# Optimization experiments

Hardware: AMD Instinct MI355X
Metric: run time of the kernel (lower is better)

The kernel has to match this reference:

```python
import jax, jax.numpy as jnp
import numpy as np

DIM = 1024
HEADS = 8
HEAD_DIM = DIM // HEADS
TAU = HEAD_DIM ** 0.5
BS, SEQ = 1, 2048


def setup_inputs() -> dict:
    key = jax.random.key(0)
    kq, kk, kv, kb = jax.random.split(key, 4)
    q = jax.random.normal(kq, (BS, SEQ, DIM), jnp.float32)
    k = jax.random.normal(kk, (BS, SEQ, DIM), jnp.float32)
    v = jax.random.normal(kv, (BS, SEQ, DIM), jnp.float32)
    Wi_w = jnp.zeros((HEADS, 3 * DIM), jnp.float32)
    Wi_b = 0.1 * jax.random.normal(kb, (HEADS,), jnp.float32)
    Wf_w = jnp.zeros((HEADS, 3 * DIM), jnp.float32)
    Wf_b = jnp.linspace(3.0, 6.0, HEADS, dtype=jnp.float32)  # equidistant_bias_init(3, 6)
    gn_w = jnp.ones((DIM,), jnp.float32)
    gn_b = jnp.zeros((DIM,), jnp.float32)
    return {"q": q, "k": k, "v": v, "Wi_w": Wi_w, "Wi_b": Wi_b,
            "Wf_w": Wf_w, "Wf_b": Wf_b, "gn_w": gn_w, "gn_b": gn_b}


def reference(q, k, v, Wi_w, Wi_b, Wf_w, Wf_b, gn_w, gn_b):
    bs, seq, dim = q.shape
    gate_in = jnp.concatenate([q, k, v], axis=-1)                    # [b, s, 3d]
    itilde = jnp.einsum('bsd,hd->bhs', gate_in, Wi_w) + Wi_b[None, :, None]
    ftilde = jnp.einsum('bsd,hd->bhs', gate_in, Wf_w) + Wf_b[None, :, None]

    # Decay matrix: F_act[i,j] = sum_{t=j+1..i} logsigmoid(ftilde_t), lower-tri else -inf
    csum = jnp.cumsum(jax.nn.log_sigmoid(ftilde), axis=-1)           # [b, h, s]
    Fmat = csum[..., :, None] - csum[..., None, :]                   # [b, h, s, s]
    mask = jnp.tril(jnp.ones((seq, seq), dtype=bool))
    F_act = jnp.where(mask, Fmat, -jnp.inf)

    Dtilde = F_act + itilde[..., None, :]                            # add input gate along j
    max_d = jnp.max(Dtilde, axis=-1, keepdims=True)
    D = jnp.exp(Dtilde - max_d)                                      # stabilized decay weights

    qh = q.reshape(bs, seq, HEADS, HEAD_DIM).transpose(0, 2, 1, 3)
    kh = k.reshape(bs, seq, HEADS, HEAD_DIM).transpose(0, 2, 1, 3)
    vh = v.reshape(bs, seq, HEADS, HEAD_DIM).transpose(0, 2, 1, 3)

    Ctilde = jnp.einsum('bhid,bhjd->bhij', qh, kh) * D / TAU
    maxit = jnp.maximum(jnp.abs(jnp.sum(Ctilde, axis=-1, keepdims=True)), jnp.exp(-max_d))
    Htilde = jnp.einsum('bhij,bhjd->bhid', Ctilde, vh) / (maxit + 1e-6)

    # GroupNorm(HEADS groups) over dim, applied per token
    x = Htilde.transpose(0, 2, 1, 3).reshape(bs * seq, HEADS, HEAD_DIM)
    mean = jnp.mean(x, axis=-1, keepdims=True)
    var = jnp.var(x, axis=-1, keepdims=True)
    xn = (x - mean) / jnp.sqrt(var + 1e-5)
    out = xn.reshape(bs * seq, DIM) * gn_w + gn_b
    return out.reshape(bs, seq, DIM)
```

## Files before the change

kernel.cpp:

```cpp
#include <hip/hip_runtime.h>
#include <math.h>

#define SEQ 2048
#define NH 8
#define HD 128
#define DIMF 1024
#define LOG2E 1.4426950408889634f
#define INVTAU 0.08838834764831845f

typedef __attribute__((ext_vector_type(8))) short bf16x8;
typedef __attribute__((ext_vector_type(8))) unsigned short us8;
typedef __attribute__((ext_vector_type(4))) float f32x4;
typedef __attribute__((ext_vector_type(16))) float f32x16;

__device__ float g_itacc[NH*SEQ];
__device__ float g_ftacc[NH*SEQ];
__device__ float g_aL[NH*SEQ];
__device__ float g_cmL[NH*SEQ];
__device__ float g_en[NH*SEQ];
__device__ unsigned short g_Qb[NH*SEQ*HD];
__device__ unsigned short g_Kb[NH*SEQ*HD];
__device__ unsigned short g_Vb[NH*SEQ*HD];
__device__ unsigned short g_Vt[NH*HD*SEQ];
__device__ unsigned short g_Wb[16*3072];

__device__ __forceinline__ unsigned short f2bf(float x) {
  unsigned u = __float_as_uint(x);
  u += 0x7fffu + ((u >> 16) & 1u);
  return (unsigned short)(u >> 16);
}

__device__ __forceinline__ unsigned packbf(float lo, float hi) {
  return (unsigned)f2bf(lo) | ((unsigned)f2bf(hi) << 16);
}

__global__ __launch_bounds__(256) void convert_kernel(const float* __restrict__ q,
                                                      const float* __restrict__ k,
                                                      const float* __restrict__ v,
                                                      const float* __restrict__ Wi,
                                                      const float* __restrict__ Wf) {
  const int bid = blockIdx.x;
  if (bid < 6144) {
    const int s = bid & 2047;
    const int t = bid >> 11;
    const float* src = (t == 0) ? q : (t == 1) ? k : v;
    unsigned short* dst = (t == 0) ? g_Qb : (t == 1) ? g_Kb : g_Vb;
    const int c = threadIdx.x * 4;
    const float4 f = *(const float4*)(src + s*DIMF + c);
    const int h = c >> 7, d = c & 127;
    ushort4 u;
    u.x = f2bf(f.x); u.y = f2bf(f.y); u.z = f2bf(f.z); u.w = f2bf(f.w);
    *(ushort4*)(dst + (h*SEQ + s)*HD + d) = u;
  } else {
    const int gid = (bid - 6144) * 256 + threadIdx.x;
    const int e4 = gid * 4;
    const int p = e4 / 3072;
    const int c = e4 % 3072;
    const float* src = (p < 8) ? (Wi + p*3072 + c) : (Wf + (p-8)*3072 + c);
    const float4 f = *(const float4*)src;
    ushort4 u;
    u.x = f2bf(f.x); u.y = f2bf(f.y); u.z = f2bf(f.z); u.w = f2bf(f.w);
    *(ushort4*)(g_Wb + p*3072 + c) = u;
  }
}

__global__ __launch_bounds__(256) void vtrans_kernel() {
  __shared__ __align__(16) unsigned short Ts[64*72];
  const int h  = blockIdx.x;
  const int s0 = blockIdx.y * 64;
  const int d0 = blockIdx.z * 64;
  const int t = threadIdx.x;
  {
    const int sr = t >> 2;
    const int c  = (t & 3) * 16;
    const unsigned short* src = g_Vb + (h*SEQ + s0 + sr)*HD + d0 + c;
    *(us8*)&Ts[sr*72 + c]     = *(const us8*)&src[0];
    *(us8*)&Ts[sr*72 + c + 8] = *(const us8*)&src[8];
  }
  __syncthreads();
  {
    const int w = t >> 6, l = t & 63;
    unsigned short outv[16];
    #pragma unroll
    for (int j = 0; j < 16; ++j) outv[j] = Ts[(w*16 + j)*72 + l];
    unsigned short* dst = g_Vt + (h*HD + d0 + l)*SEQ + s0 + w*16;
    *(us8*)&dst[0] = *(us8*)&outv[0];
    *(us8*)&dst[8] = *(us8*)&outv[8];
  }
}

__global__ __launch_bounds__(256) void gates_kernel() {
  __shared__ f32x4 red[4][64];
  const int tid = threadIdx.x;
  const int wave = tid >> 6, lane = tid & 63;
  const int q4 = lane >> 4, l16 = lane & 15;
  const int s0 = blockIdx.x * 16;
  f32x4 acc = {0.f, 0.f, 0.f, 0.f};
  #pragma unroll 8
  for (int ks = wave*24; ks < wave*24 + 24; ++ks) {
    const int k0 = ks*32 + q4*8;
    const int tsel = k0 >> 10;
    const int rem = k0 & 1023;
    const int hh = rem >> 7, dd = rem & 127;
    const unsigned short* base = (tsel == 0) ? g_Qb : (tsel == 1) ? g_Kb : g_Vb;
    const bf16x8 a = *(const bf16x8*)&base[(hh*SEQ + s0 + l16)*HD + dd];
    const bf16x8 b = *(const bf16x8*)&g_Wb[l16*3072 + k0];
    acc = __builtin_amdgcn_mfma_f32_16x16x32_bf16(a, b, acc, 0, 0, 0);
  }
  red[wave][lane] = acc;
  __syncthreads();
  if (wave == 0) {
    f32x4 s = red[0][lane];
    #pragma unroll
    for (int w = 1; w < 4; ++w) s += red[w][lane];
    #pragma unroll
    for (int r = 0; r < 4; ++r) {
      const int sg = s0 + 4*q4 + r;
      if (l16 < 8) g_itacc[l16*SEQ + sg] = s[r];
      else         g_ftacc[(l16-8)*SEQ + sg] = s[r];
    }
  }
}

__global__ __launch_bounds__(256) void scan_kernel(const float* __restrict__ Wi_b,
                                                   const float* __restrict__ Wf_b) {
  __shared__ float Wsum[4];
  __shared__ float Wmax[4];
  const int h = blockIdx.x;
  const int t = threadIdx.x;
  const int wave = t >> 6, lane = t & 63;
  const float ib = Wi_b[h];
  const float fb = Wf_b[h];
  const int base = h*SEQ + t*8;

  float it[8], ft[8];
  *(float4*)&it[0] = *(const float4*)&g_itacc[base];
  *(float4*)&it[4] = *(const float4*)&g_itacc[base+4];
  *(float4*)&ft[0] = *(const float4*)&g_ftacc[base];
  *(float4*)&ft[4] = *(const float4*)&g_ftacc[base+4];

  float cs[8];
  float run = 0.f;
  #pragma unroll
  for (int j = 0; j < 8; ++j) {
    const float f = ft[j] + fb;
    const float ls = fminf(f, 0.f) - log1pf(expf(-fabsf(f)));
    run += ls;
    cs[j] = run;
  }
  float x = run;
  #pragma unroll
  for (int off = 1; off < 64; off <<= 1) {
    const float tv = __shfl_up(x, off, 64);
    if (lane >= off) x += tv;
  }
  const float wexcl = x - run;
  if (lane == 63) Wsum[wave] = x;
  __syncthreads();
  float boff = 0.f;
  #pragma unroll
  for (int w = 0; w < 4; ++w) if (w < wave) boff += Wsum[w];
  const float cbase = boff + wexcl;

  float a[8], am[8], csum[8];
  float m = -__builtin_inff();
  #pragma unroll
  for (int j = 0; j < 8; ++j) {
    csum[j] = cbase + cs[j];
    a[j] = (it[j] + ib) - csum[j];
    m = fmaxf(m, a[j]);
    am[j] = m;
  }
  float y = m;
  #pragma unroll
  for (int off = 1; off < 64; off <<= 1) {
    const float tv = __shfl_up(y, off, 64);
    if (lane >= off) y = fmaxf(y, tv);
  }
  float e = __shfl_up(y, 1, 64);
  if (lane == 0) e = -__builtin_inff();
  if (lane == 63) Wmax[wave] = y;
  __syncthreads();
  float bmax = -__builtin_inff();
  #pragma unroll
  for (int w = 0; w < 4; ++w) if (w < wave) bmax = fmaxf(bmax, Wmax[w]);
  const float pre = fmaxf(bmax, e);

  float oa[8], ocm[8], oen[8];
  #pragma unroll
  for (int j = 0; j < 8; ++j) {
    const float cm = fmaxf(pre, am[j]);
    oa[j]  = a[j] * LOG2E;
    ocm[j] = cm * LOG2E;
    oen[j] = expf(-(csum[j] + cm));
  }
  *(float4*)&g_aL[base]    = *(float4*)&oa[0];
  *(float4*)&g_aL[base+4]  = *(float4*)&oa[4];
  *(float4*)&g_cmL[base]   = *(float4*)&ocm[0];
  *(float4*)&g_cmL[base+4] = *(float4*)&ocm[4];
  *(float4*)&g_en[base]    = *(float4*)&oen[0];
  *(float4*)&g_en[base+4]  = *(float4*)&oen[4];
}

__global__ __launch_bounds__(256, 1) void attn_kernel(const float* __restrict__ gnw,
                                                      const float* __restrict__ gnb,
                                                      float* __restrict__ out) {
  __shared__ float Osum[2][32][132];
  __shared__ float Sred[4][32];

  const int h = blockIdx.x;
  const int y = blockIdx.y;
  const int tS = y, tB = 63 - y;
  const int iS0 = 32*tS, iB0 = 32*tB;
  const int iSmax = iS0 + 31, iBmax = iB0 + 31;
  const int nvB = tB/4 + 1;

  const int tid  = threadIdx.x;
  const int w    = tid >> 6;
  const int lane = tid & 63;
  const int l31  = lane & 31;
  const int hi   = lane >> 5;

  const unsigned short* Kgh = g_Kb + (h*SEQ + l31)*HD + hi*8;
  const unsigned short* Vgh = g_Vt + (h*HD + l31)*SEQ + hi*8;
  const float*          aLh = g_aL + h*SEQ + 4*hi;

  bf16x8 qfS[8], qfB[8];
  {
    const unsigned short* QS = g_Qb + (h*SEQ + iS0 + l31)*HD + hi*8;
    const unsigned short* QB = g_Qb + (h*SEQ + iB0 + l31)*HD + hi*8;
    #pragma unroll
    for (int ks = 0; ks < 8; ++ks) {
      qfS[ks] = *(const bf16x8*)&QS[ks*16];
      qfB[ks] = *(const bf16x8*)&QB[ks*16];
    }
  }
  const float cmS = g_cmL[h*SEQ + iS0 + l31];
  const float cmB = g_cmL[h*SEQ + iB0 + l31];
  const int   igS = iS0 + l31, igB = iB0 + l31;

  f32x16 accS[4], accB[4];
  #pragma unroll
  for (int td = 0; td < 4; ++td)
    #pragma unroll
    for (int e = 0; e < 16; ++e) { accS[td][e] = 0.f; accB[td][e] = 0.f; }
  float rsS = 0.f, rsB = 0.f;

  bf16x8 Ka[8], Va[8], Kb[8], Vb[8];

  auto LOAD = [&](bf16x8 (&K)[8], bf16x8 (&V)[8], int jc) {
    const int jw = jc*128 + 32*w;
    #pragma unroll
    for (int ks = 0; ks < 8; ++ks)
      K[ks] = *(const bf16x8*)&Kgh[jw*HD + ks*16];
    #pragma unroll
    for (int td = 0; td < 4; ++td)
      #pragma unroll
      for (int ph = 0; ph < 2; ++ph)
        V[td*2 + ph] = *(const bf16x8*)&Vgh[(32*td)*SEQ + jw + 16*ph];
  };

  auto TILE = [&](int jw, const bf16x8 (&K)[8], const bf16x8 (&V)[8],
                  const float4 (&aLq)[4], const bf16x8 (&qf)[8],
                  float cm, int ig, int i0t, f32x16 (&acc)[4], float& rsum) {
    f32x16 s0a, s1a;
    #pragma unroll
    for (int e = 0; e < 16; ++e) { s0a[e] = 0.f; s1a[e] = 0.f; }
    #pragma unroll
    for (int ks = 0; ks < 8; ks += 2) {
      s0a = __builtin_amdgcn_mfma_f32_32x32x16_bf16(K[ks],   qf[ks],   s0a, 0, 0, 0);
      s1a = __builtin_amdgcn_mfma_f32_32x32x16_bf16(K[ks+1], qf[ks+1], s1a, 0, 0, 0);
    }
    const bool needMask = (jw + 31 > i0t);
    #pragma unroll
    for (int ph = 0; ph < 2; ++ph) {
      float pv[8];
      if (needMask) {
        #pragma unroll
        for (int rr = 0; rr < 8; ++rr) {
          const int r  = 8*ph + rr;
          const int rq = r >> 2;
          const float aL = ((const float*)&aLq[rq])[r & 3];
          float p = (s0a[r] + s1a[r]) * (exp2f(aL - cm) * INVTAU);
          const int jg = jw + 8*rq + 4*hi + (r & 3);
          if (jg > ig) p = 0.f;
          rsum += p;
          pv[rr] = p;
        }
      } else {
        #pragma unroll
        for (int rr = 0; rr < 8; ++rr) {
          const int r  = 8*ph + rr;
          const int rq = r >> 2;
          const float aL = ((const float*)&aLq[rq])[r & 3];
          const float p = (s0a[r] + s1a[r]) * (exp2f(aL - cm) * INVTAU);
          rsum += p;
          pv[rr] = p;
        }
      }
      const unsigned w0 = packbf(pv[0], pv[1]);
      const unsigned w1 = packbf(pv[2], pv[3]);
      const unsigned w2 = packbf(pv[4], pv[5]);
      const unsigned w3 = packbf(pv[6], pv[7]);
      const auto p0 = __builtin_amdgcn_permlane32_swap(w0, w2, false, false);
      const auto p1 = __builtin_amdgcn_permlane32_swap(w1, w3, false, false);
      union { unsigned u[4]; bf16x8 v; } fr;
      fr.u[0] = p0[0]; fr.u[1] = p1[0]; fr.u[2] = p0[1]; fr.u[3] = p1[1];
      #pragma unroll
      for (int td = 0; td < 4; ++td)
        acc[td] = __builtin_amdgcn_mfma_f32_32x32x16_bf16(fr.v, V[td*2 + ph], acc[td], 0, 0, 0);
    }
  };

  auto STEP = [&](int jc, const bf16x8 (&K)[8], const bf16x8 (&V)[8]) {
    const int jw = jc*128 + 32*w;
    float4 aLq[4];
    #pragma unroll
    for (int rq = 0; rq < 4; ++rq) aLq[rq] = *(const float4*)&aLh[jw + 8*rq];
    if (jw <= iBmax) TILE(jw, K, V, aLq, qfB, cmB, igB, iB0, accB, rsB);
    if (jw <= iSmax) TILE(jw, K, V, aLq, qfS, cmS, igS, iS0, accS, rsS);
  };

  LOAD(Ka, Va, 0);
  int jc = 0;
  for (; jc + 2 <= nvB; jc += 2) {
    LOAD(Kb, Vb, jc + 1);
    STEP(jc, Ka, Va);
    if (jc + 2 < nvB) LOAD(Ka, Va, jc + 2);
    STEP(jc + 1, Kb, Vb);
  }
  if (jc < nvB) STEP(jc, Ka, Va);

  const float* gw = gnw + h*HD;
  const float* gb = gnb + h*HD;
  auto EPI = [&](f32x16 (&acc)[4], float rsum, int i0t) {
    const float rs2 = rsum + __shfl_xor(rsum, 32, 64);
    if (hi == 0) Sred[w][l31] = rs2;
    if (w >= 2) {
      #pragma unroll
      for (int td = 0; td < 4; ++td)
        #pragma unroll
        for (int r = 0; r < 16; ++r) {
          const int row = (r & 3) + 8*(r >> 2) + 4*hi;
          Osum[w - 2][row][32*td + l31] = acc[td][r];
        }
    }
    __syncthreads();
    if (w < 2) {
      #pragma unroll
      for (int td = 0; td < 4; ++td)
        #pragma unroll
        for (int r = 0; r < 16; ++r) {
          const int row = (r & 3) + 8*(r >> 2) + 4*hi;
          Osum[w][row][32*td + l31] += acc[td][r];
        }
    }
    __syncthreads();
    const int i  = tid >> 3;
    const int d0 = (tid & 7) * 16;
    float o[16];
    #pragma unroll
    for (int e = 0; e < 16; e += 4) {
      const float4 a0 = *(const float4*)&Osum[0][i][d0 + e];
      const float4 a1 = *(const float4*)&Osum[1][i][d0 + e];
      o[e+0] = a0.x + a1.x; o[e+1] = a0.y + a1.y;
      o[e+2] = a0.z + a1.z; o[e+3] = a0.w + a1.w;
    }
    const float S  = Sred[0][i] + Sred[1][i] + Sred[2][i] + Sred[3][i];
    const float en = g_en[h*SEQ + i0t + i];
    const float sc = 1.f / (fmaxf(fabsf(S), en) + 1e-6f);
    float s1 = 0.f, s2 = 0.f;
    #pragma unroll
    for (int e = 0; e < 16; ++e) { const float xv = o[e]*sc; o[e] = xv; s1 += xv; s2 += xv*xv; }
    #pragma unroll
    for (int m = 1; m < 8; m <<= 1) { s1 += __shfl_xor(s1, m, 8); s2 += __shfl_xor(s2, m, 8); }
    const float mean = s1 * (1.f/128.f);
    const float var  = s2 * (1.f/128.f) - mean*mean;
    const float rstd = rsqrtf(var + 1e-5f);
    float* op = out + (i0t + i)*DIMF + h*HD + d0;
    #pragma unroll
    for (int e = 0; e < 16; e += 4) {
      const float4 w4 = *(const float4*)&gw[d0 + e];
      const float4 b4 = *(const float4*)&gb[d0 + e];
      float4 ov;
      ov.x = (o[e+0] - mean) * rstd * w4.x + b4.x;
      ov.y = (o[e+1] - mean) * rstd * w4.y + b4.y;
      ov.z = (o[e+2] - mean) * rstd * w4.z + b4.z;
      ov.w = (o[e+3] - mean) * rstd * w4.w + b4.w;
      *(float4*)&op[e] = ov;
    }
  };

  EPI(accS, rsS, iS0);
  __syncthreads();
  EPI(accB, rsB, iB0);
}

extern "C" void kernel_launch(void* const* d_in, const int* in_sizes, int n_in,
                              void* d_out, int out_size, void* d_ws, size_t ws_size,
                              hipStream_t stream) {
  (void)in_sizes; (void)n_in; (void)out_size; (void)d_ws; (void)ws_size;
  const float* q    = (const float*)d_in[0];
  const float* k    = (const float*)d_in[1];
  const float* v    = (const float*)d_in[2];
  const float* Wi_w = (const float*)d_in[3];
  const float* Wi_b = (const float*)d_in[4];
  const float* Wf_w = (const float*)d_in[5];
  const float* Wf_b = (const float*)d_in[6];
  const float* gnw  = (const float*)d_in[7];
  const float* gnb  = (const float*)d_in[8];
  float* out = (float*)d_out;

  convert_kernel<<<dim3(6192), 256, 0, stream>>>(q, k, v, Wi_w, Wf_w);
  vtrans_kernel<<<dim3(NH, SEQ/64, HD/64), 256, 0, stream>>>();
  gates_kernel<<<dim3(128), 256, 0, stream>>>();
  scan_kernel<<<dim3(NH), 256, 0, stream>>>(Wi_b, Wf_b);
  attn_kernel<<<dim3(NH, 32), 256, 0, stream>>>(gnw, gnb, out);
}
```

Measured before the change: 145.8 us.

## Split paired causal tiles into separate blocks and allow two blocks per CU

Each attention block now handles one 32-row query tile instead of pairing a small and a large tile, and the grid doubles to 64 tiles per head, ordered largest first. Dropping the second Q fragment and accumulator set cuts register use, and launch bounds now ask for two blocks per CU to raise occupancy. The aL vector loads are moved into the double-buffered prefetch. The cost is losing the built-in load balancing of paired tiles and K/V reuse across two query tiles, which means more global loads.

```diff
diff --git a/kernel.cpp b/kernel.cpp
--- a/kernel.cpp
+++ b/kernel.cpp
@@ -202,7 +202,7 @@
   *(float4*)&g_en[base+4]  = *(float4*)&oen[4];
 }
 
-__global__ __launch_bounds__(256, 1) void attn_kernel(const float* __restrict__ gnw,
+__global__ __launch_bounds__(256, 2) void attn_kernel(const float* __restrict__ gnw,
                                                       const float* __restrict__ gnb,
                                                       float* __restrict__ out) {
   __shared__ float Osum[2][32][132];
@@ -210,10 +210,10 @@
 
   const int h = blockIdx.x;
   const int y = blockIdx.y;
-  const int tS = y, tB = 63 - y;
-  const int iS0 = 32*tS, iB0 = 32*tB;
-  const int iSmax = iS0 + 31, iBmax = iB0 + 31;
-  const int nvB = tB/4 + 1;
+  const int t = (y < 32) ? (63 - y) : (y - 32);
+  const int i0 = 32*t;
+  const int imax = i0 + 31;
+  const int nv = (imax >> 7) + 1;
 
   const int tid  = threadIdx.x;
   const int w    = tid >> 6;
@@ -225,30 +225,26 @@
   const unsigned short* Vgh = g_Vt + (h*HD + l31)*SEQ + hi*8;
   const float*          aLh = g_aL + h*SEQ + 4*hi;
 
-  bf16x8 qfS[8], qfB[8];
+  bf16x8 qf[8];
   {
-    const unsigned short* QS = g_Qb + (h*SEQ + iS0 + l31)*HD + hi*8;
-    const unsigned short* QB = g_Qb + (h*SEQ + iB0 + l31)*HD + hi*8;
-    #pragma unroll
-    for (int ks = 0; ks < 8; ++ks) {
-      qfS[ks] = *(const bf16x8*)&QS[ks*16];
-      qfB[ks] = *(const bf16x8*)&QB[ks*16];
-    }
-  }
-  const float cmS = g_cmL[h*SEQ + iS0 + l31];
-  const float cmB = g_cmL[h*SEQ + iB0 + l31];
-  const int   igS = iS0 + l31, igB = iB0 + l31;
-
-  f32x16 accS[4], accB[4];
+    const unsigned short* Qg = g_Qb + (h*SEQ + i0 + l31)*HD + hi*8;
+    #pragma unroll
+    for (int ks = 0; ks < 8; ++ks) qf[ks] = *(const bf16x8*)&Qg[ks*16];
+  }
+  const float cm = g_cmL[h*SEQ + i0 + l31];
+  const int   ig = i0 + l31;
+
+  f32x16 acc[4];
   #pragma unroll
   for (int td = 0; td < 4; ++td)
     #pragma unroll
-    for (int e = 0; e < 16; ++e) { accS[td][e] = 0.f; accB[td][e] = 0.f; }
-  float rsS = 0.f, rsB = 0.f;
+    for (int e = 0; e < 16; ++e) acc[td][e] = 0.f;
+  float rs = 0.f;
 
   bf16x8 Ka[8], Va[8], Kb[8], Vb[8];
-
-  auto LOAD = [&](bf16x8 (&K)[8], bf16x8 (&V)[8], int jc) {
+  float4 aLa[4], aLb[4];
+
+  auto LOAD = [&](bf16x8 (&K)[8], bf16x8 (&V)[8], float4 (&A)[4], int jc) {
     const int jw = jc*128 + 32*w;
     #pragma unroll
     for (int ks = 0; ks < 8; ++ks)
@@ -258,11 +254,13 @@
       #pragma unroll
       for (int ph = 0; ph < 2; ++ph)
         V[td*2 + ph] = *(const bf16x8*)&Vgh[(32*td)*SEQ + jw + 16*ph];
+    #pragma unroll
+    for (int rq = 0; rq < 4; ++rq)
+      A[rq] = *(const float4*)&aLh[jw + 8*rq];
   };
 
   auto TILE = [&](int jw, const bf16x8 (&K)[8], const bf16x8 (&V)[8],
-                  const float4 (&aLq)[4], const bf16x8 (&qf)[8],
-                  float cm, int ig, int i0t, f32x16 (&acc)[4], float& rsum) {
+                  const float4 (&aLq)[4]) {
     f32x16 s0a, s1a;
     #pragma unroll
     for (int e = 0; e < 16; ++e) { s0a[e] = 0.f; s1a[e] = 0.f; }
@@ -271,7 +269,7 @@
       s0a = __builtin_amdgcn_mfma_f32_32x32x16_bf16(K[ks],   qf[ks],   s0a, 0, 0, 0);
       s1a = __builtin_amdgcn_mfma_f32_32x32x16_bf16(K[ks+1], qf[ks+1], s1a, 0, 0, 0);
     }
-    const bool needMask = (jw + 31 > i0t);
+    const bool needMask = (jw + 31 > i0);
     #pragma unroll
     for (int ph = 0; ph < 2; ++ph) {
       float pv[8];
@@ -284,7 +282,7 @@
           float p = (s0a[r] + s1a[r]) * (exp2f(aL - cm) * INVTAU);
           const int jg = jw + 8*rq + 4*hi + (r & 3);
           if (jg > ig) p = 0.f;
-          rsum += p;
+          rs += p;
           pv[rr] = p;
         }
       } else {
@@ -294,7 +292,7 @@
           const int rq = r >> 2;
           const float aL = ((const float*)&aLq[rq])[r & 3];
           const float p = (s0a[r] + s1a[r]) * (exp2f(aL - cm) * INVTAU);
-          rsum += p;
+          rs += p;
           pv[rr] = p;
         }
       }
@@ -312,29 +310,24 @@
     }
   };
 
-  auto STEP = [&](int jc, const bf16x8 (&K)[8], const bf16x8 (&V)[8]) {
+  auto STEP = [&](int jc, const bf16x8 (&K)[8], const bf16x8 (&V)[8],
+                  const float4 (&aLq)[4]) {
     const int jw = jc*128 + 32*w;
-    float4 aLq[4];
-    #pragma unroll
-    for (int rq = 0; rq < 4; ++rq) aLq[rq] = *(const float4*)&aLh[jw + 8*rq];
-    if (jw <= iBmax) TILE(jw, K, V, aLq, qfB, cmB, igB, iB0, accB, rsB);
-    if (jw <= iSmax) TILE(jw, K, V, aLq, qfS, cmS, igS, iS0, accS, rsS);
+    if (jw <= imax) TILE(jw, K, V, aLq);
   };
 
-  LOAD(Ka, Va, 0);
+  LOAD(Ka, Va, aLa, 0);
   int jc = 0;
-  for (; jc + 2 <= nvB; jc += 2) {
-    LOAD(Kb, Vb, jc + 1);
-    STEP(jc, Ka, Va);
-    if (jc + 2 < nvB) LOAD(Ka, Va, jc + 2);
-    STEP(jc + 1, Kb, Vb);
-  }
-  if (jc < nvB) STEP(jc, Ka, Va);
-
-  const float* gw = gnw + h*HD;
-  const float* gb = gnb + h*HD;
-  auto EPI = [&](f32x16 (&acc)[4], float rsum, int i0t) {
-    const float rs2 = rsum + __shfl_xor(rsum, 32, 64);
+  for (; jc + 2 <= nv; jc += 2) {
+    LOAD(Kb, Vb, aLb, jc + 1);
+    STEP(jc, Ka, Va, aLa);
+    if (jc + 2 < nv) LOAD(Ka, Va, aLa, jc + 2);
+    STEP(jc + 1, Kb, Vb, aLb);
+  }
+  if (jc < nv) STEP(jc, Ka, Va, aLa);
+
+  {
+    const float rs2 = rs + __shfl_xor(rs, 32, 64);
     if (hi == 0) Sred[w][l31] = rs2;
     if (w >= 2) {
       #pragma unroll
@@ -367,7 +360,7 @@
       o[e+2] = a0.z + a1.z; o[e+3] = a0.w + a1.w;
     }
     const float S  = Sred[0][i] + Sred[1][i] + Sred[2][i] + Sred[3][i];
-    const float en = g_en[h*SEQ + i0t + i];
+    const float en = g_en[h*SEQ + i0 + i];
     const float sc = 1.f / (fmaxf(fabsf(S), en) + 1e-6f);
     float s1 = 0.f, s2 = 0.f;
     #pragma unroll
@@ -377,7 +370,9 @@
     const float mean = s1 * (1.f/128.f);
     const float var  = s2 * (1.f/128.f) - mean*mean;
     const float rstd = rsqrtf(var + 1e-5f);
-    float* op = out + (i0t + i)*DIMF + h*HD + d0;
+    const float* gw = gnw + h*HD;
+    const float* gb = gnb + h*HD;
+    float* op = out + (i0 + i)*DIMF + h*HD + d0;
     #pragma unroll
     for (int e = 0; e < 16; e += 4) {
       const float4 w4 = *(const float4*)&gw[d0 + e];
@@ -389,11 +384,7 @@
       ov.w = (o[e+3] - mean) * rstd * w4.w + b4.w;
       *(float4*)&op[e] = ov;
     }
-  };
-
-  EPI(accS, rsS, iS0);
-  __syncthreads();
-  EPI(accB, rsB, iB0);
+  }
 }
 
 extern "C" void kernel_launch(void* const* d_in, const int* in_sizes, int n_in,
@@ -415,5 +406,5 @@
   vtrans_kernel<<<dim3(NH, SEQ/64, HD/64), 256, 0, stream>>>();
   gates_kernel<<<dim3(128), 256, 0, stream>>>();
   scan_kernel<<<dim3(NH), 256, 0, stream>>>(Wi_b, Wf_b);
-  attn_kernel<<<dim3(NH, 32), 256, 0, stream>>>(gnw, gnb, out);
-}
+  attn_kernel<<<dim3(NH, 64), 256, 0, stream>>>(gnw, gnb, out);
+}
```

New measurement: 192.8 us. 32.2% more time.
